# Performance work log

Measured on AMD Instinct MI355X. Metric: run time of the kernel, lower is better.

The kernel has to match this reference:

```python
import jax, jax.numpy as jnp
import numpy as np

BLOCK_SIZE = 256

def setup_inputs() -> dict:
    key = jax.random.key(0)
    ks = jax.random.split(key, 5)
    B, T, C, H = 256, 256, 512, 64
    return {
        "x": jax.random.normal(ks[0], (B, T, C), dtype=jnp.float32),
        "y": jax.random.normal(ks[1], (B, T, C), dtype=jnp.float32),
        "Wq": jax.random.normal(ks[2], (C, H), dtype=jnp.float32) * (C ** -0.5),
        "Wk": jax.random.normal(ks[3], (C, H), dtype=jnp.float32) * (C ** -0.5),
        "Wv": jax.random.normal(ks[4], (C, H), dtype=jnp.float32) * (C ** -0.5),
    }

def reference(x, y, Wq, Wk, Wv):
    # q/k/v projections (Linear without bias): [B,T,C] @ [C,H] -> [B,T,H]
    q = jnp.einsum('btc,ch->bth', x, Wq)
    k = jnp.einsum('btc,ch->bth', y, Wk)
    v = jnp.einsum('btc,ch->bth', y, Wv)
    head_size = k.shape[-1]
    # scaled dot-product scores: [B,T,T]
    wei = jnp.einsum('bth,bsh->bts', q, k) * (head_size ** -0.5)
    # causal mask (is_causal=True): lower-triangular allowed
    T = x.shape[1]
    causal = jnp.tril(jnp.ones((T, T), dtype=bool))
    wei = jnp.where(causal, wei, -jnp.inf)
    wei = jax.nn.softmax(wei, axis=-1)
    # dropout omitted (eval mode / identity)
    out = jnp.einsum('bts,bsh->bth', wei, v)
    return out
```

## Files before the change

### kernel.cpp

```cpp
#include <hip/hip_runtime.h>


typedef _Float16 half8 __attribute__((ext_vector_type(8)));
typedef float floatx4 __attribute__((ext_vector_type(4)));

#define MFMA16(a, b, c) __builtin_amdgcn_mfma_f32_16x16x32_f16((a), (b), (c), 0, 0, 0)

__device__ inline half8 cvt8(float4 a, float4 b) {
  half8 r;
  r[0] = (_Float16)a.x; r[1] = (_Float16)a.y; r[2] = (_Float16)a.z; r[3] = (_Float16)a.w;
  r[4] = (_Float16)b.x; r[5] = (_Float16)b.y; r[6] = (_Float16)b.z; r[7] = (_Float16)b.w;
  return r;
}

template <int NOUT>
__global__ __launch_bounds__(256) void proj_kernel(
    const float* __restrict__ X, const float* __restrict__ W0,
    const float* __restrict__ W1, _Float16* __restrict__ O0,
    _Float16* __restrict__ O1) {
  __shared__ _Float16 a_lds[128][40];
  __shared__ _Float16 w_lds[NOUT][64][40];

  const int tid = threadIdx.x;
  const int row0 = blockIdx.x * 128;
  const int wv = tid >> 6;
  const int lane = tid & 63;
  const int l15 = lane & 15, quad = lane >> 4;

  floatx4 acc[2][4 * NOUT];
#pragma unroll
  for (int i = 0; i < 2; i++)
#pragma unroll
    for (int j = 0; j < 4 * NOUT; j++) acc[i][j] = (floatx4)0.f;

  const int arow = tid >> 1;
  const int ahalf = (tid & 1) * 16;
  const int wkk = tid >> 3;
  const int wn0 = (tid & 7) * 8;

  for (int k0 = 0; k0 < 512; k0 += 32) {
    {
      const float4* s4 = (const float4*)(X + (size_t)(row0 + arow) * 512 + k0 + ahalf);
      float4 f0 = s4[0], f1 = s4[1], f2 = s4[2], f3 = s4[3];
      *(half8*)&a_lds[arow][ahalf]     = cvt8(f0, f1);
      *(half8*)&a_lds[arow][ahalf + 8] = cvt8(f2, f3);
    }
#pragma unroll
    for (int wi = 0; wi < NOUT; wi++) {
      const float* wsrc = (wi ? W1 : W0) + (size_t)(k0 + wkk) * 64 + wn0;
      float4 g0 = ((const float4*)wsrc)[0];
      float4 g1 = ((const float4*)wsrc)[1];
      w_lds[wi][wn0 + 0][wkk] = (_Float16)g0.x;
      w_lds[wi][wn0 + 1][wkk] = (_Float16)g0.y;
      w_lds[wi][wn0 + 2][wkk] = (_Float16)g0.z;
      w_lds[wi][wn0 + 3][wkk] = (_Float16)g0.w;
      w_lds[wi][wn0 + 4][wkk] = (_Float16)g1.x;
      w_lds[wi][wn0 + 5][wkk] = (_Float16)g1.y;
      w_lds[wi][wn0 + 6][wkk] = (_Float16)g1.z;
      w_lds[wi][wn0 + 7][wkk] = (_Float16)g1.w;
    }
    __syncthreads();
    half8 af0 = *(const half8*)&a_lds[wv * 32 + l15][quad * 8];
    half8 af1 = *(const half8*)&a_lds[wv * 32 + 16 + l15][quad * 8];
#pragma unroll
    for (int wi = 0; wi < NOUT; wi++)
#pragma unroll
      for (int j = 0; j < 4; j++) {
        half8 bf = *(const half8*)&w_lds[wi][j * 16 + l15][quad * 8];
        acc[0][wi * 4 + j] = MFMA16(af0, bf, acc[0][wi * 4 + j]);
        acc[1][wi * 4 + j] = MFMA16(af1, bf, acc[1][wi * 4 + j]);
      }
    __syncthreads();
  }
#pragma unroll
  for (int i = 0; i < 2; i++)
#pragma unroll
    for (int wi = 0; wi < NOUT; wi++) {
      _Float16* O = wi ? O1 : O0;
#pragma unroll
      for (int j = 0; j < 4; j++)
#pragma unroll
        for (int r = 0; r < 4; r++) {
          int grow = row0 + wv * 32 + i * 16 + quad * 4 + r;
          O[(size_t)grow * 64 + j * 16 + l15] = (_Float16)acc[i][wi * 4 + j][r];
        }
    }
}

__global__ __launch_bounds__(256) void attn_kernel(
    const _Float16* __restrict__ Qw, const _Float16* __restrict__ Kw,
    const _Float16* __restrict__ Vw, float* __restrict__ Out) {
  __shared__ _Float16 k_lds[64][72];
  __shared__ _Float16 vt_lds[64][72];
  __shared__ _Float16 p_lds[4][16][72];

  const int qt = blockIdx.x, bb = blockIdx.y;
  const int tid = threadIdx.x;
  const int wv = tid >> 6;
  const int lane = tid & 63;
  const int l15 = lane & 15, quad = lane >> 4;
  const float SCALE = 0.125f * 1.4426950408889634f;
  const float NEG = -3.0e38f;

  const size_t qoff = ((size_t)bb * 256 + qt * 64 + wv * 16 + l15) * 64 + quad * 8;
  half8 qf0 = *(const half8*)(Qw + qoff);
  half8 qf1 = *(const half8*)(Qw + qoff + 32);

  floatx4 o[4];
#pragma unroll
  for (int t = 0; t < 4; t++) o[t] = (floatx4)0.f;
  float mrow[4], lrow[4];
#pragma unroll
  for (int r = 0; r < 4; r++) { mrow[r] = NEG; lrow[r] = 0.f; }

  const int srow = tid >> 2;
  const int sc = (tid & 3) * 16;

  for (int j = 0; j <= qt; j++) {
    __syncthreads();
    {
      const size_t base = ((size_t)bb * 256 + j * 64 + srow) * 64 + sc;
      const half8* ksrc = (const half8*)(Kw + base);
      half8 ka = ksrc[0], kb = ksrc[1];
      *(half8*)&k_lds[srow][sc]     = ka;
      *(half8*)&k_lds[srow][sc + 8] = kb;
      const half8* vsrc = (const half8*)(Vw + base);
      half8 va = vsrc[0], vb = vsrc[1];
#pragma unroll
      for (int e = 0; e < 8; e++) vt_lds[sc + e][srow] = va[e];
#pragma unroll
      for (int e = 0; e < 8; e++) vt_lds[sc + 8 + e][srow] = vb[e];
    }
    __syncthreads();

    floatx4 sacc[4];
#pragma unroll
    for (int t = 0; t < 4; t++) sacc[t] = (floatx4)0.f;
#pragma unroll
    for (int t = 0; t < 4; t++) {
      half8 b0 = *(const half8*)&k_lds[t * 16 + l15][quad * 8];
      sacc[t] = MFMA16(qf0, b0, sacc[t]);
      half8 b1 = *(const half8*)&k_lds[t * 16 + l15][32 + quad * 8];
      sacc[t] = MFMA16(qf1, b1, sacc[t]);
    }

    float y[4][4];
#pragma unroll
    for (int t = 0; t < 4; t++)
#pragma unroll
      for (int r = 0; r < 4; r++) y[t][r] = sacc[t][r] * SCALE;
    if (j == qt) {
#pragma unroll
      for (int t = 0; t < 4; t++)
#pragma unroll
        for (int r = 0; r < 4; r++)
          if (t * 16 + l15 > wv * 16 + quad * 4 + r) y[t][r] = NEG;
    }

#pragma unroll
    for (int r = 0; r < 4; r++) {
      float mx = fmaxf(fmaxf(y[0][r], y[1][r]), fmaxf(y[2][r], y[3][r]));
#pragma unroll
      for (int off = 1; off < 16; off <<= 1) mx = fmaxf(mx, __shfl_xor(mx, off, 64));
      float mnew = fmaxf(mrow[r], mx);
      float al = exp2f(mrow[r] - mnew);
      mrow[r] = mnew;
      float rs = 0.f;
#pragma unroll
      for (int t = 0; t < 4; t++) {
        float p = exp2f(y[t][r] - mnew);
        y[t][r] = p;
        rs += p;
      }
#pragma unroll
      for (int off = 1; off < 16; off <<= 1) rs += __shfl_xor(rs, off, 64);
      lrow[r] = lrow[r] * al + rs;
      o[0][r] *= al; o[1][r] *= al; o[2][r] *= al; o[3][r] *= al;
    }

#pragma unroll
    for (int t = 0; t < 4; t++)
#pragma unroll
      for (int r = 0; r < 4; r++)
        p_lds[wv][quad * 4 + r][t * 16 + l15] = (_Float16)y[t][r];
    __syncthreads();

#pragma unroll
    for (int ss = 0; ss < 2; ss++) {
      half8 pa = *(const half8*)&p_lds[wv][l15][ss * 32 + quad * 8];
#pragma unroll
      for (int th = 0; th < 4; th++) {
        half8 vb = *(const half8*)&vt_lds[th * 16 + l15][ss * 32 + quad * 8];
        o[th] = MFMA16(pa, vb, o[th]);
      }
    }
  }

#pragma unroll
  for (int th = 0; th < 4; th++)
#pragma unroll
    for (int r = 0; r < 4; r++) {
      int grow = qt * 64 + wv * 16 + quad * 4 + r;
      Out[((size_t)bb * 256 + grow) * 64 + th * 16 + l15] = o[th][r] / lrow[r];
    }
}

extern "C" void kernel_launch(void* const* d_in, const int* in_sizes, int n_in,
                              void* d_out, int out_size, void* d_ws, size_t ws_size,
                              hipStream_t stream) {
  const float* x  = (const float*)d_in[0];
  const float* y  = (const float*)d_in[1];
  const float* Wq = (const float*)d_in[2];
  const float* Wk = (const float*)d_in[3];
  const float* Wv = (const float*)d_in[4];
  float* out = (float*)d_out;

  _Float16* qw = (_Float16*)d_ws;
  _Float16* kw = qw + (size_t)65536 * 64;
  _Float16* vw = kw + (size_t)65536 * 64;

  proj_kernel<1><<<512, 256, 0, stream>>>(x, Wq, nullptr, qw, nullptr);
  proj_kernel<2><<<512, 256, 0, stream>>>(y, Wk, Wv, kw, vw);
  attn_kernel<<<dim3(4, 256), 256, 0, stream>>>(qw, kw, vw, out);
}
```

Measured before the change: 319.8 us.

## Prepack weights to fp16 MFMA layout and merge projections into one LDS-free kernel

A new pack kernel converts Wq/Wk/Wv to fp16 once per call, in the per-lane MFMA B-fragment layout. The projection kernels are merged into a single launch that reads X/Y straight from global memory into registers with no LDS staging or barriers. The attention kernel folds the softmax scale into Q in fp16, stores V transposed into LDS as packed 32-bit pairs instead of scalar halves, and drops the barrier after the P write since each wave only reads its own P slice. Scaling Q in fp16 adds a small extra rounding error, and the direct global loads give up cross-wave reuse of the weight fragments in LDS.

```diff
diff --git a/kernel.cpp b/kernel.cpp
--- a/kernel.cpp
+++ b/kernel.cpp
@@ -13,78 +13,83 @@
   return r;
 }
 
-template <int NOUT>
-__global__ __launch_bounds__(256) void proj_kernel(
-    const float* __restrict__ X, const float* __restrict__ W0,
-    const float* __restrict__ W1, _Float16* __restrict__ O0,
-    _Float16* __restrict__ O1) {
-  __shared__ _Float16 a_lds[128][40];
-  __shared__ _Float16 w_lds[NOUT][64][40];
-
+__global__ __launch_bounds__(256) void pack_kernel(
+    const float* __restrict__ Wq, const float* __restrict__ Wk,
+    const float* __restrict__ Wv, _Float16* __restrict__ P) {
+  const int kk = blockIdx.x;
+  const int w = blockIdx.y;
+  const float* W = (w == 0) ? Wq : ((w == 1) ? Wk : Wv);
   const int tid = threadIdx.x;
-  const int row0 = blockIdx.x * 128;
-  const int wv = tid >> 6;
-  const int lane = tid & 63;
+  const int lane = tid & 63, j = tid >> 6;
   const int l15 = lane & 15, quad = lane >> 4;
-
-  floatx4 acc[2][4 * NOUT];
-#pragma unroll
-  for (int i = 0; i < 2; i++)
-#pragma unroll
-    for (int j = 0; j < 4 * NOUT; j++) acc[i][j] = (floatx4)0.f;
-
-  const int arow = tid >> 1;
-  const int ahalf = (tid & 1) * 16;
-  const int wkk = tid >> 3;
-  const int wn0 = (tid & 7) * 8;
-
-  for (int k0 = 0; k0 < 512; k0 += 32) {
-    {
-      const float4* s4 = (const float4*)(X + (size_t)(row0 + arow) * 512 + k0 + ahalf);
-      float4 f0 = s4[0], f1 = s4[1], f2 = s4[2], f3 = s4[3];
-      *(half8*)&a_lds[arow][ahalf]     = cvt8(f0, f1);
-      *(half8*)&a_lds[arow][ahalf + 8] = cvt8(f2, f3);
-    }
-#pragma unroll
-    for (int wi = 0; wi < NOUT; wi++) {
-      const float* wsrc = (wi ? W1 : W0) + (size_t)(k0 + wkk) * 64 + wn0;
-      float4 g0 = ((const float4*)wsrc)[0];
-      float4 g1 = ((const float4*)wsrc)[1];
-      w_lds[wi][wn0 + 0][wkk] = (_Float16)g0.x;
-      w_lds[wi][wn0 + 1][wkk] = (_Float16)g0.y;
-      w_lds[wi][wn0 + 2][wkk] = (_Float16)g0.z;
-      w_lds[wi][wn0 + 3][wkk] = (_Float16)g0.w;
-      w_lds[wi][wn0 + 4][wkk] = (_Float16)g1.x;
-      w_lds[wi][wn0 + 5][wkk] = (_Float16)g1.y;
-      w_lds[wi][wn0 + 6][wkk] = (_Float16)g1.z;
-      w_lds[wi][wn0 + 7][wkk] = (_Float16)g1.w;
-    }
-    __syncthreads();
-    half8 af0 = *(const half8*)&a_lds[wv * 32 + l15][quad * 8];
-    half8 af1 = *(const half8*)&a_lds[wv * 32 + 16 + l15][quad * 8];
-#pragma unroll
-    for (int wi = 0; wi < NOUT; wi++)
+  half8 h;
+#pragma unroll
+  for (int e = 0; e < 8; e++)
+    h[e] = (_Float16)W[(size_t)(kk * 32 + quad * 8 + e) * 64 + j * 16 + l15];
+  *(half8*)(P + (size_t)w * 32768 + (size_t)((kk * 4 + j) * 64 + lane) * 8) = h;
+}
+
+__global__ __launch_bounds__(256, 4) void proj_kernel(
+    const float* __restrict__ X, const float* __restrict__ Y,
+    const _Float16* __restrict__ Pw, _Float16* __restrict__ Q,
+    _Float16* __restrict__ K, _Float16* __restrict__ V) {
+  const int b = blockIdx.x;
+  const int tid = threadIdx.x;
+  const int wv = tid >> 6, lane = tid & 63;
+  const int l15 = lane & 15, quad = lane >> 4;
+  const half8* WP = (const half8*)Pw;
+
+  if (b < 1024) {
+    const int row0 = b * 64;
+    const float* A = X + (size_t)(row0 + wv * 16 + l15) * 512 + quad * 8;
+    floatx4 acc[4];
+#pragma unroll
+    for (int j = 0; j < 4; j++) acc[j] = (floatx4)0.f;
+#pragma unroll
+    for (int kk = 0; kk < 16; kk++) {
+      float4 a0 = *(const float4*)(A + kk * 32);
+      float4 a1 = *(const float4*)(A + kk * 32 + 4);
+      half8 af = cvt8(a0, a1);
 #pragma unroll
       for (int j = 0; j < 4; j++) {
-        half8 bf = *(const half8*)&w_lds[wi][j * 16 + l15][quad * 8];
-        acc[0][wi * 4 + j] = MFMA16(af0, bf, acc[0][wi * 4 + j]);
-        acc[1][wi * 4 + j] = MFMA16(af1, bf, acc[1][wi * 4 + j]);
-      }
-    __syncthreads();
+        half8 bf = WP[(kk * 4 + j) * 64 + lane];
+        acc[j] = MFMA16(af, bf, acc[j]);
+      }
+    }
+#pragma unroll
+    for (int j = 0; j < 4; j++)
+#pragma unroll
+      for (int r = 0; r < 4; r++)
+        Q[(size_t)(row0 + wv * 16 + quad * 4 + r) * 64 + j * 16 + l15] =
+            (_Float16)acc[j][r];
+  } else {
+    const int row0 = (b - 1024) * 64;
+    const float* A = Y + (size_t)(row0 + wv * 16 + l15) * 512 + quad * 8;
+    floatx4 acck[4], accv[4];
+#pragma unroll
+    for (int j = 0; j < 4; j++) { acck[j] = (floatx4)0.f; accv[j] = (floatx4)0.f; }
+#pragma unroll
+    for (int kk = 0; kk < 16; kk++) {
+      float4 a0 = *(const float4*)(A + kk * 32);
+      float4 a1 = *(const float4*)(A + kk * 32 + 4);
+      half8 af = cvt8(a0, a1);
+#pragma unroll
+      for (int j = 0; j < 4; j++) {
+        half8 bk = WP[4096 + (kk * 4 + j) * 64 + lane];
+        acck[j] = MFMA16(af, bk, acck[j]);
+        half8 bv = WP[8192 + (kk * 4 + j) * 64 + lane];
+        accv[j] = MFMA16(af, bv, accv[j]);
+      }
+    }
+#pragma unroll
+    for (int j = 0; j < 4; j++)
+#pragma unroll
+      for (int r = 0; r < 4; r++) {
+        const size_t o = (size_t)(row0 + wv * 16 + quad * 4 + r) * 64 + j * 16 + l15;
+        K[o] = (_Float16)acck[j][r];
+        V[o] = (_Float16)accv[j][r];
+      }
   }
-#pragma unroll
-  for (int i = 0; i < 2; i++)
-#pragma unroll
-    for (int wi = 0; wi < NOUT; wi++) {
-      _Float16* O = wi ? O1 : O0;
-#pragma unroll
-      for (int j = 0; j < 4; j++)
-#pragma unroll
-        for (int r = 0; r < 4; r++) {
-          int grow = row0 + wv * 32 + i * 16 + quad * 4 + r;
-          O[(size_t)grow * 64 + j * 16 + l15] = (_Float16)acc[i][wi * 4 + j][r];
-        }
-    }
 }
 
 __global__ __launch_bounds__(256) void attn_kernel(
@@ -99,12 +104,14 @@
   const int wv = tid >> 6;
   const int lane = tid & 63;
   const int l15 = lane & 15, quad = lane >> 4;
-  const float SCALE = 0.125f * 1.4426950408889634f;
   const float NEG = -3.0e38f;
+  const _Float16 SCALE = (_Float16)(0.125f * 1.4426950408889634f);
 
   const size_t qoff = ((size_t)bb * 256 + qt * 64 + wv * 16 + l15) * 64 + quad * 8;
   half8 qf0 = *(const half8*)(Qw + qoff);
   half8 qf1 = *(const half8*)(Qw + qoff + 32);
+#pragma unroll
+  for (int e = 0; e < 8; e++) { qf0[e] *= SCALE; qf1[e] *= SCALE; }
 
   floatx4 o[4];
 #pragma unroll
@@ -115,21 +122,27 @@
 
   const int srow = tid >> 2;
   const int sc = (tid & 3) * 16;
+  const int sp = tid & 31;
+  const int h0 = (tid >> 5) * 8;
+  unsigned int* vt32 = (unsigned int*)&vt_lds[0][0];
 
   for (int j = 0; j <= qt; j++) {
     __syncthreads();
     {
-      const size_t base = ((size_t)bb * 256 + j * 64 + srow) * 64 + sc;
-      const half8* ksrc = (const half8*)(Kw + base);
+      const size_t kbase = ((size_t)bb * 256 + j * 64 + srow) * 64 + sc;
+      const half8* ksrc = (const half8*)(Kw + kbase);
       half8 ka = ksrc[0], kb = ksrc[1];
       *(half8*)&k_lds[srow][sc]     = ka;
       *(half8*)&k_lds[srow][sc + 8] = kb;
-      const half8* vsrc = (const half8*)(Vw + base);
-      half8 va = vsrc[0], vb = vsrc[1];
-#pragma unroll
-      for (int e = 0; e < 8; e++) vt_lds[sc + e][srow] = va[e];
-#pragma unroll
-      for (int e = 0; e < 8; e++) vt_lds[sc + 8 + e][srow] = vb[e];
+      const _Float16* vsrc = Vw + ((size_t)bb * 256 + j * 64 + 2 * sp) * 64 + h0;
+      half8 va = *(const half8*)vsrc;
+      half8 vb = *(const half8*)(vsrc + 64);
+#pragma unroll
+      for (int e = 0; e < 8; e++) {
+        union { _Float16 h[2]; unsigned int u; } pk;
+        pk.h[0] = va[e]; pk.h[1] = vb[e];
+        vt32[(h0 + e) * 36 + sp] = pk.u;
+      }
     }
     __syncthreads();
 
@@ -148,7 +161,7 @@
 #pragma unroll
     for (int t = 0; t < 4; t++)
 #pragma unroll
-      for (int r = 0; r < 4; r++) y[t][r] = sacc[t][r] * SCALE;
+      for (int r = 0; r < 4; r++) y[t][r] = sacc[t][r];
     if (j == qt) {
 #pragma unroll
       for (int t = 0; t < 4; t++)
@@ -183,7 +196,6 @@
 #pragma unroll
       for (int r = 0; r < 4; r++)
         p_lds[wv][quad * 4 + r][t * 16 + l15] = (_Float16)y[t][r];
-    __syncthreads();
 
 #pragma unroll
     for (int ss = 0; ss < 2; ss++) {
@@ -218,8 +230,9 @@
   _Float16* qw = (_Float16*)d_ws;
   _Float16* kw = qw + (size_t)65536 * 64;
   _Float16* vw = kw + (size_t)65536 * 64;
-
-  proj_kernel<1><<<512, 256, 0, stream>>>(x, Wq, nullptr, qw, nullptr);
-  proj_kernel<2><<<512, 256, 0, stream>>>(y, Wk, Wv, kw, vw);
+  _Float16* wpack = vw + (size_t)65536 * 64;
+
+  pack_kernel<<<dim3(16, 3), 256, 0, stream>>>(Wq, Wk, Wv, wpack);
+  proj_kernel<<<2048, 256, 0, stream>>>(x, y, wpack, qw, kw, vw);
   attn_kernel<<<dim3(4, 256), 256, 0, stream>>>(qw, kw, vw, out);
 }
```

After: 331.6 us. +3.7%, slower.
